# Kernel optimization log

Measured on AMD Instinct MI355X. Metric: run time of the kernel, lower is better.

Reference implementation:

```python
import jax, jax.numpy as jnp
import numpy as np

NUM_BUCKETS = 14
SCALE_FACTOR = 3.0
MAX_SHAPE = (800, 1333)  # (H, W)
SIDE = int(np.ceil(NUM_BUCKETS / 2.0))  # 7
B, N = 8, 131072


def setup_inputs() -> dict:
    key = jax.random.key(0)
    k1, k2, k3, k4, kc, ko = jax.random.split(key, 6)
    # valid xyxy proposals inside a ~1333x800 image
    x1 = jax.random.uniform(k1, (B, N)) * 1000.0
    y1 = jax.random.uniform(k2, (B, N)) * 600.0
    w = jax.random.uniform(k3, (B, N)) * 300.0 + 16.0
    h = jax.random.uniform(k4, (B, N)) * 300.0 + 16.0
    proposals = jnp.stack([x1, y1, x1 + w, y1 + h], axis=-1)
    cls_preds = jax.random.normal(kc, (B, N * 4 * SIDE), dtype=jnp.float32)
    offset_preds = jax.random.normal(ko, (B, N * 4 * SIDE), dtype=jnp.float32) * 0.5
    return {"proposals": proposals, "cls_preds": cls_preds, "offset_preds": offset_preds}


def reference(proposals, cls_preds, offset_preds):
    batch = cls_preds.shape[0]
    cls = cls_preds.reshape(batch, -1, SIDE)                 # [B, 4N, S]
    scores = jax.nn.softmax(cls, axis=2)
    score_topk, score_label = jax.lax.top_k(scores, 2)      # [B, 4N, 2]

    # bbox_rescale: scale w/h about the box center
    cx = (proposals[..., 0] + proposals[..., 2]) * 0.5
    cy = (proposals[..., 1] + proposals[..., 3]) * 0.5
    pw = (proposals[..., 2] - proposals[..., 0]) * SCALE_FACTOR
    ph = (proposals[..., 3] - proposals[..., 1]) * SCALE_FACTOR
    px1 = cx - 0.5 * pw
    py1 = cy - 0.5 * ph
    px2 = cx + 0.5 * pw
    py2 = cy + 0.5 * ph
    bucket_w = pw / NUM_BUCKETS
    bucket_h = ph / NUM_BUCKETS

    # rows are interleaved (l, r, t, d) per proposal
    inds_l = score_label[:, 0::4, 0]
    inds_r = score_label[:, 1::4, 0]
    inds_t = score_label[:, 2::4, 0]
    inds_d = score_label[:, 3::4, 0]

    f32 = jnp.float32
    l_buckets = px1 + (0.5 + inds_l.astype(f32)) * bucket_w
    r_buckets = px2 - (0.5 + inds_r.astype(f32)) * bucket_w
    t_buckets = py1 + (0.5 + inds_t.astype(f32)) * bucket_h
    d_buckets = py2 - (0.5 + inds_d.astype(f32)) * bucket_h

    offsets = offset_preds.reshape(batch, -1, 4, SIDE)       # [B, N, 4, S]
    l_off = jnp.take_along_axis(offsets[:, :, 0, :], inds_l[..., None], axis=2)[..., 0]
    r_off = jnp.take_along_axis(offsets[:, :, 1, :], inds_r[..., None], axis=2)[..., 0]
    t_off = jnp.take_along_axis(offsets[:, :, 2, :], inds_t[..., None], axis=2)[..., 0]
    d_off = jnp.take_along_axis(offsets[:, :, 3, :], inds_d[..., None], axis=2)[..., 0]

    x1 = l_buckets - l_off * bucket_w
    x2 = r_buckets - r_off * bucket_w
    y1 = t_buckets - t_off * bucket_h
    y2 = d_buckets - d_off * bucket_h

    H, W = MAX_SHAPE
    x1 = jnp.clip(x1, 0.0, W - 1)
    y1 = jnp.clip(y1, 0.0, H - 1)
    x2 = jnp.clip(x2, 0.0, W - 1)
    y2 = jnp.clip(y2, 0.0, H - 1)
    bboxes = jnp.stack([x1, y1, x2, y2], axis=-1)            # [B, N, 4]

    loc_conf = score_topk[:, :, 0]
    top2_neighbor = jnp.abs((score_label[:, :, 0] - score_label[:, :, 1]).astype(f32)) - 1.0
    loc_conf = loc_conf + score_topk[:, :, 1] * top2_neighbor
    loc_conf = loc_conf.reshape(batch, -1, 4).mean(axis=2)   # [B, N]
    return bboxes, loc_conf
```

## Files before the change

kernel.cpp:

```cpp
#include <hip/hip_runtime.h>
#include <math.h>


#define SIDE_N 7

__global__ __launch_bounds__(256) void bucketing_bbox_kernel(
    const float* __restrict__ proposals,
    const float* __restrict__ cls_preds,
    const float* __restrict__ offset_preds,
    float* __restrict__ out_bboxes,
    float* __restrict__ out_conf,
    int total)
{
    int i = blockIdx.x * blockDim.x + threadIdx.x;
    if (i >= total) return;

    float4 pr = reinterpret_cast<const float4*>(proposals)[i];

    float cls[28];
    float offs[28];
    {
        const float4* cp = reinterpret_cast<const float4*>(cls_preds + (size_t)i * 28);
        const float4* op = reinterpret_cast<const float4*>(offset_preds + (size_t)i * 28);
        float4* cd = reinterpret_cast<float4*>(cls);
        float4* od = reinterpret_cast<float4*>(offs);
#pragma unroll
        for (int k = 0; k < 7; ++k) cd[k] = cp[k];
#pragma unroll
        for (int k = 0; k < 7; ++k) od[k] = op[k];
    }

    float cx = (pr.x + pr.z) * 0.5f;
    float cy = (pr.y + pr.w) * 0.5f;
    float pw = (pr.z - pr.x) * 3.0f;
    float ph = (pr.w - pr.y) * 3.0f;
    float px1 = cx - 0.5f * pw;
    float px2 = cx + 0.5f * pw;
    float py1 = cy - 0.5f * ph;
    float py2 = cy + 0.5f * ph;
    float bw = pw / 14.0f;
    float bh = ph / 14.0f;

    int   lab0s[4];
    float offsel[4];
    float conf_sum = 0.0f;

#pragma unroll
    for (int s = 0; s < 4; ++s) {
        float best0 = cls[s * SIDE_N + 0];
        float best1 = -INFINITY;
        int   lab0 = 0, lab1 = 0;
        float osel = offs[s * SIDE_N + 0];
#pragma unroll
        for (int j = 1; j < SIDE_N; ++j) {
            float x = cls[s * SIDE_N + j];
            float o = offs[s * SIDE_N + j];
            bool gt0 = x > best0;
            bool gt1 = x > best1;
            best1 = gt0 ? best0 : (gt1 ? x : best1);
            lab1  = gt0 ? lab0  : (gt1 ? j : lab1);
            best0 = gt0 ? x : best0;
            lab0  = gt0 ? j : lab0;
            osel  = gt0 ? o : osel;
        }
        float sum = 0.0f;
#pragma unroll
        for (int j = 0; j < SIDE_N; ++j) {
            sum += __expf(cls[s * SIDE_N + j] - best0);
        }
        float inv = 1.0f / sum;
        float p0 = inv;
        float p1 = __expf(best1 - best0) * inv;

        lab0s[s]  = lab0;
        offsel[s] = osel;

        float neighbor = fabsf((float)(lab0 - lab1)) - 1.0f;
        conf_sum += p0 + p1 * neighbor;
    }

    float l_b = px1 + (0.5f + (float)lab0s[0]) * bw;
    float r_b = px2 - (0.5f + (float)lab0s[1]) * bw;
    float t_b = py1 + (0.5f + (float)lab0s[2]) * bh;
    float d_b = py2 - (0.5f + (float)lab0s[3]) * bh;

    float x1 = l_b - offsel[0] * bw;
    float x2 = r_b - offsel[1] * bw;
    float y1 = t_b - offsel[2] * bh;
    float y2 = d_b - offsel[3] * bh;

    const float Wm = 1332.0f;
    const float Hm = 799.0f;
    x1 = fminf(fmaxf(x1, 0.0f), Wm);
    x2 = fminf(fmaxf(x2, 0.0f), Wm);
    y1 = fminf(fmaxf(y1, 0.0f), Hm);
    y2 = fminf(fmaxf(y2, 0.0f), Hm);

    float4 box = make_float4(x1, y1, x2, y2);
    reinterpret_cast<float4*>(out_bboxes)[i] = box;
    out_conf[i] = conf_sum * 0.25f;
}

extern "C" void kernel_launch(void* const* d_in, const int* in_sizes, int n_in,
                              void* d_out, int out_size, void* d_ws, size_t ws_size,
                              hipStream_t stream) {
    const float* proposals    = (const float*)d_in[0];
    const float* cls_preds    = (const float*)d_in[1];
    const float* offset_preds = (const float*)d_in[2];

    int total = in_sizes[0] / 4;

    float* out_bboxes = (float*)d_out;
    float* out_conf   = (float*)d_out + (size_t)total * 4;

    int block = 256;
    int grid = (total + block - 1) / block;
    bucketing_bbox_kernel<<<grid, block, 0, stream>>>(
        proposals, cls_preds, offset_preds, out_bboxes, out_conf, total);
}
```

Baseline: 263.3 us.

## Stage cls and offset loads through padded LDS for coalesced global reads

```diff
diff --git a/kernel.cpp b/kernel.cpp
--- a/kernel.cpp
+++ b/kernel.cpp
@@ -2,33 +2,106 @@
 #include <math.h>
 
 
-#define SIDE_N 7
-
-__global__ __launch_bounds__(256) void bucketing_bbox_kernel(
+#define TILE 256
+#define PAD_ROW 29
+
+__global__ __launch_bounds__(256) void bucketing_bbox_tile_kernel(
     const float* __restrict__ proposals,
     const float* __restrict__ cls_preds,
     const float* __restrict__ offset_preds,
     float* __restrict__ out_bboxes,
-    float* __restrict__ out_conf,
-    int total)
+    float* __restrict__ out_conf)
 {
-    int i = blockIdx.x * blockDim.x + threadIdx.x;
-    if (i >= total) return;
-
-    float4 pr = reinterpret_cast<const float4*>(proposals)[i];
+    __shared__ float lds[TILE * PAD_ROW];
+
+    const int t = threadIdx.x;
+    const size_t base = (size_t)blockIdx.x * TILE;
+    const size_t gid = base + t;
+
+    const float4* clsv = reinterpret_cast<const float4*>(cls_preds) + base * 7;
+    const float4* offv = reinterpret_cast<const float4*>(offset_preds) + base * 7;
+    float4 creg[7], oreg[7];
+#pragma unroll
+    for (int k = 0; k < 7; ++k) creg[k] = clsv[t + TILE * k];
+#pragma unroll
+    for (int k = 0; k < 7; ++k) oreg[k] = offv[t + TILE * k];
+    float4 pr = reinterpret_cast<const float4*>(proposals)[gid];
+
+    const int p0 = t / 7;
+    const int e0 = t - p0 * 7;
+
+    {
+        int p = p0, e = e0;
+#pragma unroll
+        for (int k = 0; k < 7; ++k) {
+            int a = p * PAD_ROW + 4 * e;
+            lds[a + 0] = creg[k].x;
+            lds[a + 1] = creg[k].y;
+            lds[a + 2] = creg[k].z;
+            lds[a + 3] = creg[k].w;
+            p += 36; e += 4;
+            if (e >= 7) { e -= 7; p += 1; }
+        }
+    }
+    __syncthreads();
 
     float cls[28];
-    float offs[28];
-    {
-        const float4* cp = reinterpret_cast<const float4*>(cls_preds + (size_t)i * 28);
-        const float4* op = reinterpret_cast<const float4*>(offset_preds + (size_t)i * 28);
-        float4* cd = reinterpret_cast<float4*>(cls);
-        float4* od = reinterpret_cast<float4*>(offs);
-#pragma unroll
-        for (int k = 0; k < 7; ++k) cd[k] = cp[k];
-#pragma unroll
-        for (int k = 0; k < 7; ++k) od[k] = op[k];
-    }
+    {
+        const int rb = t * PAD_ROW;
+#pragma unroll
+        for (int j = 0; j < 28; ++j) cls[j] = lds[rb + j];
+    }
+
+    int   lab0s[4];
+    float conf_sum = 0.0f;
+#pragma unroll
+    for (int s = 0; s < 4; ++s) {
+        float best0 = cls[s * 7 + 0];
+        float best1 = -INFINITY;
+        int   lab0 = 0, lab1 = 0;
+#pragma unroll
+        for (int j = 1; j < 7; ++j) {
+            float x = cls[s * 7 + j];
+            bool gt0 = x > best0;
+            bool gt1 = x > best1;
+            best1 = gt0 ? best0 : (gt1 ? x : best1);
+            lab1  = gt0 ? lab0  : (gt1 ? j : lab1);
+            best0 = gt0 ? x : best0;
+            lab0  = gt0 ? j : lab0;
+        }
+        float sum = 0.0f;
+#pragma unroll
+        for (int j = 0; j < 7; ++j) sum += __expf(cls[s * 7 + j] - best0);
+        float inv = 1.0f / sum;
+        float p0s = inv;
+        float p1s = __expf(best1 - best0) * inv;
+
+        lab0s[s] = lab0;
+        float neighbor = fabsf((float)(lab0 - lab1)) - 1.0f;
+        conf_sum += p0s + p1s * neighbor;
+    }
+    __syncthreads();
+
+    {
+        int p = p0, e = e0;
+#pragma unroll
+        for (int k = 0; k < 7; ++k) {
+            int a = p * PAD_ROW + 4 * e;
+            lds[a + 0] = oreg[k].x;
+            lds[a + 1] = oreg[k].y;
+            lds[a + 2] = oreg[k].z;
+            lds[a + 3] = oreg[k].w;
+            p += 36; e += 4;
+            if (e >= 7) { e -= 7; p += 1; }
+        }
+    }
+    __syncthreads();
+
+    const int rb = t * PAD_ROW;
+    float osel0 = lds[rb + 0  + lab0s[0]];
+    float osel1 = lds[rb + 7  + lab0s[1]];
+    float osel2 = lds[rb + 14 + lab0s[2]];
+    float osel3 = lds[rb + 21 + lab0s[3]];
 
     float cx = (pr.x + pr.z) * 0.5f;
     float cy = (pr.y + pr.w) * 0.5f;
@@ -41,53 +114,15 @@
     float bw = pw / 14.0f;
     float bh = ph / 14.0f;
 
-    int   lab0s[4];
-    float offsel[4];
-    float conf_sum = 0.0f;
-
-#pragma unroll
-    for (int s = 0; s < 4; ++s) {
-        float best0 = cls[s * SIDE_N + 0];
-        float best1 = -INFINITY;
-        int   lab0 = 0, lab1 = 0;
-        float osel = offs[s * SIDE_N + 0];
-#pragma unroll
-        for (int j = 1; j < SIDE_N; ++j) {
-            float x = cls[s * SIDE_N + j];
-            float o = offs[s * SIDE_N + j];
-            bool gt0 = x > best0;
-            bool gt1 = x > best1;
-            best1 = gt0 ? best0 : (gt1 ? x : best1);
-            lab1  = gt0 ? lab0  : (gt1 ? j : lab1);
-            best0 = gt0 ? x : best0;
-            lab0  = gt0 ? j : lab0;
-            osel  = gt0 ? o : osel;
-        }
-        float sum = 0.0f;
-#pragma unroll
-        for (int j = 0; j < SIDE_N; ++j) {
-            sum += __expf(cls[s * SIDE_N + j] - best0);
-        }
-        float inv = 1.0f / sum;
-        float p0 = inv;
-        float p1 = __expf(best1 - best0) * inv;
-
-        lab0s[s]  = lab0;
-        offsel[s] = osel;
-
-        float neighbor = fabsf((float)(lab0 - lab1)) - 1.0f;
-        conf_sum += p0 + p1 * neighbor;
-    }
-
     float l_b = px1 + (0.5f + (float)lab0s[0]) * bw;
     float r_b = px2 - (0.5f + (float)lab0s[1]) * bw;
     float t_b = py1 + (0.5f + (float)lab0s[2]) * bh;
     float d_b = py2 - (0.5f + (float)lab0s[3]) * bh;
 
-    float x1 = l_b - offsel[0] * bw;
-    float x2 = r_b - offsel[1] * bw;
-    float y1 = t_b - offsel[2] * bh;
-    float y2 = d_b - offsel[3] * bh;
+    float x1 = l_b - osel0 * bw;
+    float x2 = r_b - osel1 * bw;
+    float y1 = t_b - osel2 * bh;
+    float y2 = d_b - osel3 * bh;
 
     const float Wm = 1332.0f;
     const float Hm = 799.0f;
@@ -96,8 +131,71 @@
     y1 = fminf(fmaxf(y1, 0.0f), Hm);
     y2 = fminf(fmaxf(y2, 0.0f), Hm);
 
-    float4 box = make_float4(x1, y1, x2, y2);
-    reinterpret_cast<float4*>(out_bboxes)[i] = box;
+    reinterpret_cast<float4*>(out_bboxes)[gid] = make_float4(x1, y1, x2, y2);
+    out_conf[gid] = conf_sum * 0.25f;
+}
+
+__global__ __launch_bounds__(256) void bucketing_bbox_tail_kernel(
+    const float* __restrict__ proposals,
+    const float* __restrict__ cls_preds,
+    const float* __restrict__ offset_preds,
+    float* __restrict__ out_bboxes,
+    float* __restrict__ out_conf,
+    int start, int total)
+{
+    int i = start + blockIdx.x * blockDim.x + threadIdx.x;
+    if (i >= total) return;
+
+    float4 pr = reinterpret_cast<const float4*>(proposals)[i];
+    float cls[28], offs[28];
+    {
+        const float4* cp = reinterpret_cast<const float4*>(cls_preds + (size_t)i * 28);
+        const float4* op = reinterpret_cast<const float4*>(offset_preds + (size_t)i * 28);
+#pragma unroll
+        for (int k = 0; k < 7; ++k) reinterpret_cast<float4*>(cls)[k] = cp[k];
+#pragma unroll
+        for (int k = 0; k < 7; ++k) reinterpret_cast<float4*>(offs)[k] = op[k];
+    }
+    float cx = (pr.x + pr.z) * 0.5f;
+    float cy = (pr.y + pr.w) * 0.5f;
+    float pw = (pr.z - pr.x) * 3.0f;
+    float ph = (pr.w - pr.y) * 3.0f;
+    float px1 = cx - 0.5f * pw, px2 = cx + 0.5f * pw;
+    float py1 = cy - 0.5f * ph, py2 = cy + 0.5f * ph;
+    float bw = pw / 14.0f, bh = ph / 14.0f;
+
+    int lab0s[4]; float offsel[4]; float conf_sum = 0.0f;
+#pragma unroll
+    for (int s = 0; s < 4; ++s) {
+        float best0 = cls[s * 7], best1 = -INFINITY;
+        int lab0 = 0, lab1 = 0;
+        float osel = offs[s * 7];
+#pragma unroll
+        for (int j = 1; j < 7; ++j) {
+            float x = cls[s * 7 + j], o = offs[s * 7 + j];
+            bool gt0 = x > best0, gt1 = x > best1;
+            best1 = gt0 ? best0 : (gt1 ? x : best1);
+            lab1  = gt0 ? lab0  : (gt1 ? j : lab1);
+            best0 = gt0 ? x : best0;
+            lab0  = gt0 ? j : lab0;
+            osel  = gt0 ? o : osel;
+        }
+        float sum = 0.0f;
+#pragma unroll
+        for (int j = 0; j < 7; ++j) sum += __expf(cls[s * 7 + j] - best0);
+        float inv = 1.0f / sum;
+        lab0s[s] = lab0; offsel[s] = osel;
+        conf_sum += inv + __expf(best1 - best0) * inv * (fabsf((float)(lab0 - lab1)) - 1.0f);
+    }
+    float x1 = px1 + (0.5f + (float)lab0s[0]) * bw - offsel[0] * bw;
+    float x2 = px2 - (0.5f + (float)lab0s[1]) * bw - offsel[1] * bw;
+    float y1 = py1 + (0.5f + (float)lab0s[2]) * bh - offsel[2] * bh;
+    float y2 = py2 - (0.5f + (float)lab0s[3]) * bh - offsel[3] * bh;
+    x1 = fminf(fmaxf(x1, 0.0f), 1332.0f);
+    x2 = fminf(fmaxf(x2, 0.0f), 1332.0f);
+    y1 = fminf(fmaxf(y1, 0.0f), 799.0f);
+    y2 = fminf(fmaxf(y2, 0.0f), 799.0f);
+    reinterpret_cast<float4*>(out_bboxes)[i] = make_float4(x1, y1, x2, y2);
     out_conf[i] = conf_sum * 0.25f;
 }
 
@@ -113,8 +211,16 @@
     float* out_bboxes = (float*)d_out;
     float* out_conf   = (float*)d_out + (size_t)total * 4;
 
-    int block = 256;
-    int grid = (total + block - 1) / block;
-    bucketing_bbox_kernel<<<grid, block, 0, stream>>>(
-        proposals, cls_preds, offset_preds, out_bboxes, out_conf, total);
+    int full_tiles = total / TILE;
+    int rem = total - full_tiles * TILE;
+
+    if (full_tiles > 0) {
+        bucketing_bbox_tile_kernel<<<full_tiles, TILE, 0, stream>>>(
+            proposals, cls_preds, offset_preds, out_bboxes, out_conf);
+    }
+    if (rem > 0) {
+        int start = full_tiles * TILE;
+        bucketing_bbox_tail_kernel<<<(rem + 255) / 256, 256, 0, stream>>>(
+            proposals, cls_preds, offset_preds, out_bboxes, out_conf, start, total);
+    }
 }
```

Measured after the change: 261.0 us. Within noise of the previous version (-0.9%).
